# Kernel optimization log

Measured on AMD Instinct MI355X. Metric: run time of the kernel, lower is better.

The kernel has to match this reference:

```python
import jax, jax.numpy as jnp
import numpy as np

N_NODES = 10000
N_EDGES = 160000
D = 512
HID = 512
N_LAYERS = 3
N_CLASSES = 10
N_GRAPHS = 64


def setup_inputs() -> dict:
    key = jax.random.key(0)
    ks = jax.random.split(key, 8)
    x = jax.random.normal(ks[0], (N_NODES, D), dtype=jnp.float32)
    edge_index = jax.random.randint(ks[1], (2, N_EDGES), 0, N_NODES, dtype=jnp.int64)
    batch = jnp.sort(jax.random.randint(ks[2], (N_NODES,), 0, N_GRAPHS, dtype=jnp.int64))
    # GCNConv weights (in == hid == 512 for all layers, so stack them)
    scale_w = 1.0 / np.sqrt(HID)
    Ws = jax.random.normal(ks[3], (N_LAYERS, HID, HID), dtype=jnp.float32) * scale_w
    bs = jnp.zeros((N_LAYERS, HID), dtype=jnp.float32)
    lin_w = jax.random.normal(ks[4], (HID, N_CLASSES), dtype=jnp.float32) * scale_w
    lin_b = jnp.zeros((N_CLASSES,), dtype=jnp.float32)
    return {"x": x, "edge_index": edge_index, "batch": batch,
            "Ws": Ws, "bs": bs, "lin_w": lin_w, "lin_b": lin_b}


def reference(x, edge_index, batch, Ws, bs, lin_w, lin_b):
    N = x.shape[0]
    # GCNConv: add self-loops, symmetric deg^-1/2 normalization (computed once,
    # since the graph is fixed across layers)
    loops = jnp.arange(N, dtype=edge_index.dtype)
    row = jnp.concatenate([edge_index[0], loops])  # source
    col = jnp.concatenate([edge_index[1], loops])  # target (aggregation index)
    deg = jax.ops.segment_sum(jnp.ones_like(col, dtype=x.dtype), col, num_segments=N)
    dinv = jax.lax.rsqrt(deg)  # deg >= 1 thanks to self-loops
    norm = (dinv[row] * dinv[col])[:, None]  # [E+N, 1]

    for i in range(Ws.shape[0]):
        h = x @ Ws[i]                                   # [N, HID] dense transform
        out = jax.ops.segment_sum(h[row] * norm, col, num_segments=N)
        x = jax.nn.relu(out + bs[i])
        # dropout(p=0.5) is identity in eval mode

    pooled = jax.ops.segment_sum(x, batch, num_segments=N_GRAPHS)  # [G, HID]
    logits = pooled @ lin_w + lin_b                                 # [G, C]
    return jax.nn.log_softmax(logits, axis=1)
```

## Files before the change

### kernel.cpp

```cpp
#include <hip/hip_runtime.h>

#define N_NODES 10000
#define HID 512
#define MPAD 10112
#define N_GRAPHS 64
#define N_CLASSES 10

typedef __bf16 bf16_t;
typedef __bf16 bf16x8 __attribute__((ext_vector_type(8)));
typedef float  f32x4  __attribute__((ext_vector_type(4)));

__device__ __forceinline__ void gload16(const bf16_t* g, bf16_t* l) {
    __builtin_amdgcn_global_load_lds(
        (const __attribute__((address_space(1))) void*)g,
        (__attribute__((address_space(3))) void*)l,
        16, 0, 0);
}

__global__ void zero_k(int* __restrict__ cnt, int* __restrict__ cur,
                       bf16_t* __restrict__ xh_pad, bf16_t* __restrict__ xl_pad,
                       float* __restrict__ pooled) {
    int i = blockIdx.x * 256 + threadIdx.x;
    if (i < N_NODES) { cnt[i] = 0; cur[i] = 0; }
    const int PCH = (MPAD - N_NODES) * HID / 8;
    uint4 z = {0, 0, 0, 0};
    if (i < PCH) {
        *(uint4*)&xh_pad[i * 8] = z;
        *(uint4*)&xl_pad[i * 8] = z;
    }
    if (i < N_GRAPHS * HID / 4) *(uint4*)&pooled[i * 4] = z;
}

#define CVX_B 2500
#define CVW_B 3072
__global__ void setup_k(const float* __restrict__ x,
                        bf16_t* __restrict__ xh, bf16_t* __restrict__ xl,
                        const float* __restrict__ W, bf16_t* __restrict__ whT,
                        const int* __restrict__ ecol, int* __restrict__ cnt, int E) {
    int b = blockIdx.x, t = threadIdx.x;
    if (b < CVX_B) {
        int idx = (b * 256 + t) * 8;
        f32x4 v0 = *(const f32x4*)&x[idx];
        f32x4 v1 = *(const f32x4*)&x[idx + 4];
        float v[8] = {v0[0], v0[1], v0[2], v0[3], v1[0], v1[1], v1[2], v1[3]};
        bf16x8 hi, lo;
#pragma unroll
        for (int j = 0; j < 8; ++j) {
            bf16_t h = (bf16_t)v[j];
            hi[j] = h;
            lo[j] = (bf16_t)(v[j] - (float)h);
        }
        *(bf16x8*)&xh[idx] = hi;
        *(bf16x8*)&xl[idx] = lo;
    } else if (b < CVX_B + CVW_B) {
        int o   = (b - CVX_B) * 256 + t;
        int lyr = o >> 18;
        int rem = o & 262143;
        int j   = rem >> 9;
        int k   = rem & 511;
        whT[o] = (bf16_t)W[(lyr << 18) + (k << 9) + j];
    } else {
        int e = (b - CVX_B - CVW_B) * 256 + t;
        if (e < E) atomicAdd(&cnt[ecol[e]], 1);
    }
}

__global__ __launch_bounds__(1024) void scan_k(const int* __restrict__ cnt,
                                               int* __restrict__ off,
                                               float* __restrict__ dinv) {
    __shared__ int s[1024];
    int t = threadIdx.x;
    int base = t * 10;
    int loc[10];
    int sum = 0;
#pragma unroll
    for (int j = 0; j < 10; ++j) {
        int n = base + j;
        int v = (n < N_NODES) ? cnt[n] : 0;
        if (n < N_NODES) dinv[n] = rsqrtf(1.0f + (float)v);
        loc[j] = sum;
        sum += v;
    }
    s[t] = sum;
    __syncthreads();
    for (int o = 1; o < 1024; o <<= 1) {
        int v = (t >= o) ? s[t - o] : 0;
        __syncthreads();
        s[t] += v;
        __syncthreads();
    }
    int pre = (t > 0) ? s[t - 1] : 0;
#pragma unroll
    for (int j = 0; j < 10; ++j) {
        int n = base + j;
        if (n <= N_NODES) off[n] = pre + loc[j];
    }
}

__global__ void scatter_k(const int* __restrict__ row, const int* __restrict__ col,
                          const int* __restrict__ off, int* __restrict__ cursor,
                          const float* __restrict__ dinv,
                          int2* __restrict__ epk, int E) {
    int e = blockIdx.x * 256 + threadIdx.x;
    if (e >= E) return;
    int c = col[e], r = row[e];
    int p = off[c] + atomicAdd(&cursor[c], 1);
    float w = dinv[r] * dinv[c];
    epk[p] = make_int2(r, __float_as_int(w));
}

__global__ __launch_bounds__(256) void gemm3(
    const bf16_t* __restrict__ xh, const bf16_t* __restrict__ xl,
    const bf16_t* __restrict__ wh,
    bf16_t* __restrict__ hh)
{
    __shared__ alignas(16) bf16_t sAh[2][64 * 32];
    __shared__ alignas(16) bf16_t sAl[2][64 * 32];
    __shared__ alignas(16) bf16_t sBh[2][128 * 32];

    const int t  = threadIdx.x;
    const int l  = t & 63;
    const int wv = t >> 6;
    const int wr = wv >> 1;
    const int wc = wv & 1;
    const int n0 = blockIdx.x * 128;
    const int m0 = blockIdx.y * 64;

    f32x4 acc[2][4];
#pragma unroll
    for (int m = 0; m < 2; ++m)
#pragma unroll
        for (int n = 0; n < 4; ++n) acc[m][n] = (f32x4){0.f, 0.f, 0.f, 0.f};

    const int lr  = l & 15;
    const int kgr = (l >> 4) * 8;
    const int srow = t >> 2;
    const int sce  = (t & 3) * 8;

    auto stage = [&](int buf, int kk) {
        size_t gA  = (size_t)(m0 + srow) * HID + kk + sce;
        size_t gB0 = (size_t)(n0 + srow) * HID + kk + sce;
        size_t gB1 = (size_t)(n0 + 64 + srow) * HID + kk + sce;
        gload16(&xh[gA],  &sAh[buf][t * 8]);
        gload16(&xl[gA],  &sAl[buf][t * 8]);
        gload16(&wh[gB0], &sBh[buf][t * 8]);
        gload16(&wh[gB1], &sBh[buf][(t + 256) * 8]);
    };

    stage(0, 0);
    __syncthreads();

    int cur = 0;
    for (int kk = 0; kk < HID; kk += 32) {
        if (kk + 32 < HID) stage(cur ^ 1, kk + 32);

        bf16x8 ah[2], al[2], bh[4];
#pragma unroll
        for (int m = 0; m < 2; ++m) {
            int row = wr * 32 + m * 16 + lr;
            ah[m] = *(const bf16x8*)&sAh[cur][row * 32 + kgr];
            al[m] = *(const bf16x8*)&sAl[cur][row * 32 + kgr];
        }
#pragma unroll
        for (int n = 0; n < 4; ++n) {
            int col = wc * 64 + n * 16 + lr;
            bh[n] = *(const bf16x8*)&sBh[cur][col * 32 + kgr];
        }
#pragma unroll
        for (int m = 0; m < 2; ++m)
#pragma unroll
            for (int n = 0; n < 4; ++n) {
                acc[m][n] = __builtin_amdgcn_mfma_f32_16x16x32_bf16(ah[m], bh[n], acc[m][n], 0, 0, 0);
                acc[m][n] = __builtin_amdgcn_mfma_f32_16x16x32_bf16(al[m], bh[n], acc[m][n], 0, 0, 0);
            }

        __syncthreads();
        cur ^= 1;
    }

    const int rq = (l >> 4) * 4;
#pragma unroll
    for (int m = 0; m < 2; ++m) {
        int row = m0 + wr * 32 + m * 16 + rq;
#pragma unroll
        for (int n = 0; n < 4; ++n) {
            int col = n0 + wc * 64 + n * 16 + lr;
#pragma unroll
            for (int r = 0; r < 4; ++r)
                hh[(size_t)(row + r) * HID + col] = (bf16_t)acc[m][n][r];
        }
    }
}

template <bool LAST>
__global__ __launch_bounds__(256) void agg_k(
    const bf16_t* __restrict__ hh, const int* __restrict__ off,
    const int2* __restrict__ epk,
    const float* __restrict__ dinv, const float* __restrict__ bias,
    bf16_t* __restrict__ xh, bf16_t* __restrict__ xl, float* __restrict__ x3)
{
    int node = blockIdx.x * 4 + (threadIdx.x >> 6);
    if (node >= N_NODES) return;
    int l  = threadIdx.x & 63;
    int c0 = l * 8;

    float dn = dinv[node];
    float sw = dn * dn;
    float a[8];
    {
        bf16x8 sv = *(const bf16x8*)&hh[(size_t)node * HID + c0];
#pragma unroll
        for (int j = 0; j < 8; ++j) a[j] = (float)sv[j] * sw;
    }

    int e0 = off[node], e1 = off[node + 1];
    int e = e0;
    for (; e + 4 <= e1; e += 4) {
        int4 p0 = *(const int4*)&epk[e];
        int4 p1 = *(const int4*)&epk[e + 2];
        bf16x8 v0 = *(const bf16x8*)&hh[(size_t)p0.x * HID + c0];
        bf16x8 v1 = *(const bf16x8*)&hh[(size_t)p0.z * HID + c0];
        bf16x8 v2 = *(const bf16x8*)&hh[(size_t)p1.x * HID + c0];
        bf16x8 v3 = *(const bf16x8*)&hh[(size_t)p1.z * HID + c0];
        float w0 = __int_as_float(p0.y), w1 = __int_as_float(p0.w);
        float w2 = __int_as_float(p1.y), w3 = __int_as_float(p1.w);
#pragma unroll
        for (int j = 0; j < 8; ++j) {
            a[j] += (float)v0[j] * w0 + (float)v1[j] * w1
                  + (float)v2[j] * w2 + (float)v3[j] * w3;
        }
    }
    for (; e < e1; ++e) {
        int2 ed = epk[e];
        float w = __int_as_float(ed.y);
        bf16x8 v = *(const bf16x8*)&hh[(size_t)ed.x * HID + c0];
#pragma unroll
        for (int j = 0; j < 8; ++j) a[j] += (float)v[j] * w;
    }
#pragma unroll
    for (int j = 0; j < 8; ++j) {
        a[j] += bias[c0 + j];
        if (a[j] < 0.f) a[j] = 0.f;
    }

    if (LAST) {
        f32x4 o0 = {a[0], a[1], a[2], a[3]};
        f32x4 o1 = {a[4], a[5], a[6], a[7]};
        *(f32x4*)&x3[(size_t)node * HID + c0]     = o0;
        *(f32x4*)&x3[(size_t)node * HID + c0 + 4] = o1;
    } else {
        bf16x8 hi, lo;
#pragma unroll
        for (int j = 0; j < 8; ++j) {
            bf16_t hb = (bf16_t)a[j];
            hi[j] = hb;
            lo[j] = (bf16_t)(a[j] - (float)hb);
        }
        *(bf16x8*)&xh[(size_t)node * HID + c0] = hi;
        *(bf16x8*)&xl[(size_t)node * HID + c0] = lo;
    }
}

__global__ void pool_k(const float* __restrict__ x3, const int* __restrict__ batch,
                       float* __restrict__ pooled) {
    int t  = threadIdx.x;
    int n0 = blockIdx.x * 20;
    int nend = min(n0 + 20, N_NODES);
    float acc0 = 0.f, acc1 = 0.f;
    int cur = -1;
    for (int n = n0; n < nend; ++n) {
        int g = batch[n];
        if (g != cur) {
            if (cur >= 0) {
                atomicAdd(&pooled[cur * HID + t], acc0);
                atomicAdd(&pooled[cur * HID + t + 256], acc1);
            }
            cur = g; acc0 = 0.f; acc1 = 0.f;
        }
        acc0 += x3[(size_t)n * HID + t];
        acc1 += x3[(size_t)n * HID + t + 256];
    }
    if (cur >= 0) {
        atomicAdd(&pooled[cur * HID + t], acc0);
        atomicAdd(&pooled[cur * HID + t + 256], acc1);
    }
}

__global__ __launch_bounds__(64) void head_k(const float* __restrict__ pooled,
                                             const float* __restrict__ lw,
                                             const float* __restrict__ lb,
                                             float* __restrict__ out) {
    int g = blockIdx.x, l = threadIdx.x;
    float lg[10];
#pragma unroll
    for (int c = 0; c < N_CLASSES; ++c) {
        float s = 0.f;
        for (int k = l; k < HID; k += 64) s += pooled[g * HID + k] * lw[k * N_CLASSES + c];
        for (int o2 = 32; o2 > 0; o2 >>= 1) s += __shfl_down(s, o2);
        lg[c] = s;
    }
    if (l == 0) {
        float mx = -1e30f;
#pragma unroll
        for (int c = 0; c < N_CLASSES; ++c) { lg[c] += lb[c]; mx = fmaxf(mx, lg[c]); }
        float se = 0.f;
#pragma unroll
        for (int c = 0; c < N_CLASSES; ++c) se += expf(lg[c] - mx);
        float lse = logf(se);
#pragma unroll
        for (int c = 0; c < N_CLASSES; ++c) out[g * N_CLASSES + c] = lg[c] - mx - lse;
    }
}

extern "C" void kernel_launch(void* const* d_in, const int* in_sizes, int n_in,
                              void* d_out, int out_size, void* d_ws, size_t ws_size,
                              hipStream_t stream) {
    const float* x     = (const float*)d_in[0];
    const int*   ei    = (const int*)d_in[1];
    const int*   batch = (const int*)d_in[2];
    const float* Ws    = (const float*)d_in[3];
    const float* bs    = (const float*)d_in[4];
    const float* lw    = (const float*)d_in[5];
    const float* lb    = (const float*)d_in[6];
    float*       out   = (float*)d_out;
    const int E = in_sizes[1] / 2;
    const int* erow = ei;
    const int* ecol = ei + E;

    char* p = (char*)d_ws;
    auto take = [&](size_t bytes) {
        char* q = p;
        p += (bytes + 255) & ~(size_t)255;
        return q;
    };
    bf16_t* xh    = (bf16_t*)take((size_t)MPAD * HID * 2);
    bf16_t* xl    = (bf16_t*)take((size_t)MPAD * HID * 2);
    bf16_t* hh    = (bf16_t*)take((size_t)MPAD * HID * 2);
    float*  x3    = (float*) take((size_t)N_NODES * HID * 4);
    bf16_t* whT   = (bf16_t*)take((size_t)3 * HID * HID * 2);
    float*  dinv  = (float*) take((size_t)N_NODES * 4);
    int*    cnt   = (int*)   take((size_t)N_NODES * 4);
    int*    off   = (int*)   take((size_t)(N_NODES + 1) * 4);
    int*    cur   = (int*)   take((size_t)N_NODES * 4);
    int2*   epk   = (int2*)  take((size_t)E * 8 + 16);
    float*  pooled= (float*) take((size_t)N_GRAPHS * HID * 4);

    const int cdeg_b = (E + 255) / 256;
    zero_k<<<40, 256, 0, stream>>>(cnt, cur, xh + (size_t)N_NODES * HID,
                                   xl + (size_t)N_NODES * HID, pooled);
    setup_k<<<CVX_B + CVW_B + cdeg_b, 256, 0, stream>>>(
        x, xh, xl, Ws, whT, ecol, cnt, E);
    scan_k<<<1, 1024, 0, stream>>>(cnt, off, dinv);
    scatter_k<<<cdeg_b, 256, 0, stream>>>(erow, ecol, off, cur, dinv, epk, E);

    for (int lyr = 0; lyr < 3; ++lyr) {
        gemm3<<<dim3(4, 158), 256, 0, stream>>>(
            xh, xl, whT + (size_t)lyr * HID * HID, hh);
        if (lyr < 2)
            agg_k<false><<<(N_NODES + 3) / 4, 256, 0, stream>>>(
                hh, off, epk, dinv, bs + lyr * HID, xh, xl, nullptr);
        else
            agg_k<true><<<(N_NODES + 3) / 4, 256, 0, stream>>>(
                hh, off, epk, dinv, bs + lyr * HID, nullptr, nullptr, x3);
    }
    pool_k<<<500, 256, 0, stream>>>(x3, batch, pooled);
    head_k<<<N_GRAPHS, 64, 0, stream>>>(pooled, lw, lb, out);
}
```

Measured before the change: 195.8 us.

## Triple-buffer GEMM LDS tiles with explicit vmcnt waits and raw barriers

Changes the GEMM K-loop from double to triple buffering in LDS. Two tiles are prefetched ahead, and partial s_waitcnt vmcnt counts let the next tile's async global-to-LDS loads stay in flight while the current tile is computed. Raw s_barrier calls with manual waitcnt replace __syncthreads. This is meant to hide global load latency better, at the cost of 50% more LDS per block, which may reduce occupancy, and of relying on hand-counted vmcnt values.

```diff
diff --git a/kernel.cpp b/kernel.cpp
--- a/kernel.cpp
+++ b/kernel.cpp
@@ -114,9 +114,9 @@
     const bf16_t* __restrict__ wh,
     bf16_t* __restrict__ hh)
 {
-    __shared__ alignas(16) bf16_t sAh[2][64 * 32];
-    __shared__ alignas(16) bf16_t sAl[2][64 * 32];
-    __shared__ alignas(16) bf16_t sBh[2][128 * 32];
+    __shared__ alignas(16) bf16_t sAh[3][64 * 32];
+    __shared__ alignas(16) bf16_t sAl[3][64 * 32];
+    __shared__ alignas(16) bf16_t sBh[3][128 * 32];
 
     const int t  = threadIdx.x;
     const int l  = t & 63;
@@ -147,24 +147,18 @@
         gload16(&wh[gB1], &sBh[buf][(t + 256) * 8]);
     };
 
-    stage(0, 0);
-    __syncthreads();
-
-    int cur = 0;
-    for (int kk = 0; kk < HID; kk += 32) {
-        if (kk + 32 < HID) stage(cur ^ 1, kk + 32);
-
+    auto compute = [&](int buf) {
         bf16x8 ah[2], al[2], bh[4];
 #pragma unroll
         for (int m = 0; m < 2; ++m) {
             int row = wr * 32 + m * 16 + lr;
-            ah[m] = *(const bf16x8*)&sAh[cur][row * 32 + kgr];
-            al[m] = *(const bf16x8*)&sAl[cur][row * 32 + kgr];
+            ah[m] = *(const bf16x8*)&sAh[buf][row * 32 + kgr];
+            al[m] = *(const bf16x8*)&sAl[buf][row * 32 + kgr];
         }
 #pragma unroll
         for (int n = 0; n < 4; ++n) {
             int col = wc * 64 + n * 16 + lr;
-            bh[n] = *(const bf16x8*)&sBh[cur][col * 32 + kgr];
+            bh[n] = *(const bf16x8*)&sBh[buf][col * 32 + kgr];
         }
 #pragma unroll
         for (int m = 0; m < 2; ++m)
@@ -173,9 +167,36 @@
                 acc[m][n] = __builtin_amdgcn_mfma_f32_16x16x32_bf16(ah[m], bh[n], acc[m][n], 0, 0, 0);
                 acc[m][n] = __builtin_amdgcn_mfma_f32_16x16x32_bf16(al[m], bh[n], acc[m][n], 0, 0, 0);
             }
-
-        __syncthreads();
-        cur ^= 1;
+    };
+
+    stage(0, 0);
+    stage(1, 32);
+
+    const int NT = HID / 32;
+    for (int i = 0; i < NT - 2; ++i) {
+        __builtin_amdgcn_s_barrier();
+        asm volatile("" ::: "memory");
+        stage((i + 2) % 3, (i + 2) * 32);
+        asm volatile("s_waitcnt vmcnt(8)" ::: "memory");
+        __builtin_amdgcn_s_barrier();
+        asm volatile("" ::: "memory");
+        compute(i % 3);
+    }
+    {
+        __builtin_amdgcn_s_barrier();
+        asm volatile("" ::: "memory");
+        asm volatile("s_waitcnt vmcnt(4)" ::: "memory");
+        __builtin_amdgcn_s_barrier();
+        asm volatile("" ::: "memory");
+        compute((NT - 2) % 3);
+    }
+    {
+        __builtin_amdgcn_s_barrier();
+        asm volatile("" ::: "memory");
+        asm volatile("s_waitcnt vmcnt(0)" ::: "memory");
+        __builtin_amdgcn_s_barrier();
+        asm volatile("" ::: "memory");
+        compute((NT - 1) % 3);
     }
 
     const int rq = (l >> 4) * 4;
```

New measurement: 200.1 us. +2.2%, slower.
